# Performance work log

Measured on AMD Instinct MI355X. Metric: run time of the kernel, lower is better.

## Reference

```python
import jax, jax.numpy as jnp
import numpy as np

N, F, E, FE, H, OUT = 20000, 128, 320000, 16, 128, 128
NTYPES = 2  # types = (0, 1)
NPAIRS = NTYPES * NTYPES


def setup_inputs() -> dict:
    key = jax.random.key(0)
    ks = jax.random.split(key, 12)
    edge_in_dim = 2 * F + FE
    node_in_dim = F + H
    s = lambda *shape: 1.0 / np.sqrt(shape[-2])
    return {
        "x": jax.random.normal(ks[0], (N, 1, F), dtype=jnp.float32),
        "edge_index": jax.random.randint(ks[1], (2, E), 0, N, dtype=jnp.int64),
        "edge_attr": jax.random.normal(ks[2], (E, FE), dtype=jnp.float32),
        "node_type": jax.random.randint(ks[3], (N,), 0, NTYPES, dtype=jnp.int64),
        # edge MLP params, stacked over the 4 (t1,t2) type pairs
        "ew1": jax.random.normal(ks[4], (NPAIRS, edge_in_dim, H), dtype=jnp.float32) * (1.0 / np.sqrt(edge_in_dim)),
        "eb1": jnp.zeros((NPAIRS, H), dtype=jnp.float32),
        "ew2": jax.random.normal(ks[5], (NPAIRS, H, H), dtype=jnp.float32) * (1.0 / np.sqrt(H)),
        "eb2": jnp.zeros((NPAIRS, H), dtype=jnp.float32),
        # node MLP params, stacked over the 2 node types
        "nw1": jax.random.normal(ks[6], (NTYPES, node_in_dim, H), dtype=jnp.float32) * (1.0 / np.sqrt(node_in_dim)),
        "nb1": jnp.zeros((NTYPES, H), dtype=jnp.float32),
        "nw2": jax.random.normal(ks[7], (NTYPES, H, OUT), dtype=jnp.float32) * (1.0 / np.sqrt(H)),
        "nb2": jnp.zeros((NTYPES, OUT), dtype=jnp.float32),
    }


def reference(x, edge_index, edge_attr, node_type, ew1, eb1, ew2, eb2, nw1, nb1, nw2, nb2):
    x0 = x[:, 0]  # [N, F]
    row, col = edge_index[0], edge_index[1]

    # ---- edge model: type-pair-dispatched 2-layer ReLU MLP ----
    edge_in = jnp.concatenate([x0[row], x0[col], edge_attr], axis=-1)  # [E, 2F+FE]
    h1 = jax.nn.relu(jnp.einsum("ei,pih->eph", edge_in, ew1) + eb1)    # [E, P, H]
    h2 = jax.nn.relu(jnp.einsum("eph,phk->epk", h1, ew2) + eb2)        # [E, P, H]
    pair_id = node_type[row] * NTYPES + node_type[col]                  # [E]
    pair_oh = jax.nn.one_hot(pair_id, NPAIRS, dtype=h2.dtype)           # [E, P]
    edge_feat = jnp.einsum("epk,ep->ek", h2, pair_oh)                   # [E, H]

    # ---- aggregation: sum over incoming edges per source (row) node ----
    agg = jax.ops.segment_sum(edge_feat, row, num_segments=N)           # [N, H]

    # ---- node model: type-dispatched 2-layer MLP + residual ----
    node_in = jnp.concatenate([x0, agg], axis=-1)                       # [N, F+H]
    n1 = jax.nn.relu(jnp.einsum("ni,tih->nth", node_in, nw1) + nb1)     # [N, T, H]
    n2 = jnp.einsum("nth,thk->ntk", n1, nw2) + nb2                      # [N, T, OUT]
    type_oh = jax.nn.one_hot(node_type, NTYPES, dtype=n2.dtype)         # [N, T]
    out = jnp.einsum("ntk,nt->nk", n2, type_oh)                         # [N, OUT]
    out = out + x0[:, :OUT]  # residual
    return out[:, None, :]  # [N, 1, OUT]
```

## Files before the change

### kernel.cpp

```cpp
#include <hip/hip_runtime.h>

#define N_NODES 20000
#define N_EDGES 320000
#define NBINS   (4*N_NODES)
#define SCAN_NBLK 313
#define PRECONV_NBLK 11216
#define HIST_NBLK 1250

typedef unsigned short u16;
typedef __attribute__((ext_vector_type(8))) short bf16x8;
typedef __attribute__((ext_vector_type(4))) float f32x4;
typedef __attribute__((ext_vector_type(4))) unsigned int u32x4;
typedef __attribute__((ext_vector_type(2))) unsigned int u32x2;

__device__ __forceinline__ float b2f(u16 b){
  unsigned u = ((unsigned)b) << 16; float f; __builtin_memcpy(&f, &u, 4); return f;
}
__device__ __forceinline__ u16 f2b(float f){
  unsigned u; __builtin_memcpy(&u, &f, 4); u += 0x7FFF + ((u >> 16) & 1); return (u16)(u >> 16);
}
__device__ __forceinline__ unsigned cvtpk(float a, float b){
  unsigned r;
  asm("v_cvt_pk_bf16_f32 %0, %1, %2" : "=v"(r) : "v"(a), "v"(b));
  return r;
}

#define NX   (N_NODES*128)
#define NW1T (4*288*128)
#define NW2T (4*128*128)
#define NN1  (2*256*128)
#define NN2  (2*128*128)

__global__ void k_prep(const float* __restrict__ x,
                       const float* __restrict__ ew1, const float* __restrict__ ew2,
                       const float* __restrict__ nw1, const float* __restrict__ nw2,
                       u16* __restrict__ x0b,
                       u16* __restrict__ wt1t, u16* __restrict__ wt2t,
                       u16* __restrict__ nw1t, u16* __restrict__ nw2t,
                       const int* __restrict__ ei, const int* __restrict__ ntp,
                       int* __restrict__ hist, int* __restrict__ hist_nt,
                       u16* __restrict__ srank)
{
  int bid = blockIdx.x;
  if (bid >= PRECONV_NBLK) {
    int t = (bid - PRECONV_NBLK) * 256 + threadIdx.x;
    int lane = threadIdx.x & 63;
    if (t < N_EDGES) {
      int r = ei[t], c = ei[N_EDGES + t];
      int tr = ntp[r], tc = ntp[c];
      int key = (tr * 2 + tc) * N_NODES + r;
      int rk = atomicAdd(&hist[key], 1);
      srank[t] = (u16)rk;
    }
    bool valid = t < N_NODES;
    int ty = valid ? ntp[t] : -1;
    unsigned long long m0 = __ballot(ty == 0);
    unsigned long long m1 = __ballot(ty == 1);
    if (lane == 0) {
      int c0 = __popcll(m0), c1 = __popcll(m1);
      if (c0) atomicAdd(&hist_nt[0], c0);
      if (c1) atomicAdd(&hist_nt[1], c1);
    }
    return;
  }
  int t = bid * 256 + threadIdx.x;
  if (t < NX) { x0b[t] = f2b(x[t]); return; }
  t -= NX;
  if (t < NW1T) {
    int p = t / 36864, r = t % 36864; int k = r >> 7, n = r & 127;
    float v = (k < 272) ? ew1[(p * 272 + k) * 128 + n] : 0.f;
    wt1t[(p * 128 + n) * 288 + k] = f2b(v);
    return;
  }
  t -= NW1T;
  if (t < NW2T) {
    int p = t >> 14, r = t & 16383; int k = r >> 7, n = r & 127;
    wt2t[(p * 128 + n) * 128 + k] = f2b(ew2[(p * 128 + k) * 128 + n]);
    return;
  }
  t -= NW2T;
  if (t < NN1) {
    int ty = t >> 15, r = t & 32767; int k = r >> 7, n = r & 127;
    nw1t[(ty * 128 + n) * 256 + k] = f2b(nw1[(ty * 256 + k) * 128 + n]);
    return;
  }
  t -= NN1;
  if (t < NN2) {
    int ty = t >> 14, r = t & 16383; int k = r >> 7, n = r & 127;
    nw2t[(ty * 128 + n) * 128 + k] = f2b(nw2[(ty * 128 + k) * 128 + n]);
  }
}

__global__ void k_scan1(const int* __restrict__ hist, int* __restrict__ parts)
{
  __shared__ int s[256];
  int i = blockIdx.x * 256 + threadIdx.x;
  s[threadIdx.x] = (i < NBINS) ? hist[i] : 0;
  __syncthreads();
  for (int off = 128; off > 0; off >>= 1) {
    if (threadIdx.x < off) s[threadIdx.x] += s[threadIdx.x + off];
    __syncthreads();
  }
  if (threadIdx.x == 0) parts[blockIdx.x] = s[0];
}

__global__ void k_scan2(int* __restrict__ parts)
{
  __shared__ int s[512];
  int t = threadIdx.x;
  int v = (t < SCAN_NBLK) ? parts[t] : 0;
  s[t] = v; __syncthreads();
  for (int off = 1; off < 512; off <<= 1) {
    int xv = (t >= off) ? s[t - off] : 0;
    __syncthreads();
    s[t] += xv;
    __syncthreads();
  }
  if (t < SCAN_NBLK) parts[t] = s[t] - v;
}

__global__ void k_scan3(const int* __restrict__ hist, const int* __restrict__ parts,
                        int* __restrict__ bstart)
{
  __shared__ int s[256];
  int i = blockIdx.x * 256 + threadIdx.x;
  int v = (i < NBINS) ? hist[i] : 0;
  s[threadIdx.x] = v; __syncthreads();
  for (int off = 1; off < 256; off <<= 1) {
    int xv = (threadIdx.x >= off) ? s[threadIdx.x - off] : 0;
    __syncthreads();
    s[threadIdx.x] += xv;
    __syncthreads();
  }
  int excl = s[threadIdx.x] - v + parts[blockIdx.x];
  if (i < NBINS) bstart[i] = excl;
  if (i == 0) bstart[NBINS] = N_EDGES;
}

__global__ void k_place(const int* __restrict__ ei, const int* __restrict__ ntp,
                        const u16* __restrict__ srank, const int* __restrict__ bstart,
                        int2* __restrict__ sedge,
                        int* __restrict__ cur_nt, const int* __restrict__ hist_nt,
                        int* __restrict__ nidx)
{
  int t = blockIdx.x * 256 + threadIdx.x;
  int lane = threadIdx.x & 63;
  if (t < N_EDGES) {
    int r = ei[t], c = ei[N_EDGES + t];
    int tr = ntp[r], tc = ntp[c];
    int key = (tr * 2 + tc) * N_NODES + r;
    int pos = bstart[key] + (int)srank[t];
    int2 v; v.x = r | (c << 15); v.y = t;
    sedge[pos] = v;
  }
  bool valid = t < N_NODES;
  int ty = valid ? ntp[t] : -1;
  unsigned long long m0 = __ballot(ty == 0);
  unsigned long long m1 = __ballot(ty == 1);
  int b0 = 0, b1 = 0;
  if (lane == 0) {
    int c0 = __popcll(m0), c1 = __popcll(m1);
    if (c0) b0 = atomicAdd(&cur_nt[0], c0);
    if (c1) b1 = atomicAdd(&cur_nt[1], c1);
  }
  b0 = __shfl(b0, 0); b1 = __shfl(b1, 0);
  if (valid) {
    unsigned long long lt = (1ull << lane) - 1ull;
    int pos = (ty == 0) ? (b0 + __popcll(m0 & lt))
                        : (hist_nt[0] + b1 + __popcll(m1 & lt));
    nidx[pos] = t;
  }
}

__launch_bounds__(512, 2)
__global__ void k_edge(const u16* __restrict__ x0b, const float* __restrict__ ea,
                       const u16* __restrict__ wt1t, const u16* __restrict__ wt2t,
                       const float* __restrict__ eb1, const float* __restrict__ eb2,
                       const int* __restrict__ bstart, const int2* __restrict__ sedge,
                       u16* __restrict__ h2s)
{
  __shared__ u16 sW1[36 * 1024];
  __shared__ u16 sW2[16 * 1024];
  __shared__ u16 slab[8][16 * 128];
  __shared__ float sEb1[128];
  __shared__ float sEb2[128];

  const int p    = blockIdx.y;
  const int tid  = threadIdx.x;
  const int lane = tid & 63;
  const int wv   = tid >> 6;
  const int llo  = lane & 15;
  const int lhi  = lane >> 4;

  const int base_p = bstart[p * N_NODES];
  const int end_p  = bstart[(p + 1) * N_NODES];

  for (int i = tid; i < 128 * 36; i += 512) {
    int n = i / 36, c = i % 36;
    *(u32x4*)&sW1[(c * 128 + n) * 8] = *(const u32x4*)&wt1t[(p * 128 + n) * 288 + c * 8];
  }
  for (int i = tid; i < 128 * 16; i += 512) {
    int n = i >> 4, c = i & 15;
    *(u32x4*)&sW2[(c * 128 + n) * 8] = *(const u32x4*)&wt2t[(p * 128 + n) * 128 + c * 8];
  }
  if (tid < 128) sEb1[tid] = eb1[p * 128 + tid];
  else if (tid < 256) sEb2[tid - 128] = eb2[p * 128 + tid - 128];
  __syncthreads();

  u16* myslab = &slab[wv][0];
  const int stride = gridDim.x * 256;
  const int ts0 = base_p + blockIdx.x * 256;

  int2 mN0 = {0, 0}, mN1 = {0, 0};
  if (ts0 < end_p) {
    const int e0 = ts0 + wv * 32;
    int q0 = e0 + llo;       q0 = q0 < end_p ? q0 : end_p - 1;
    int q1 = e0 + 16 + llo;  q1 = q1 < end_p ? q1 : end_p - 1;
    mN0 = sedge[q0];
    mN1 = sedge[q1];
  }

  for (int ts = ts0; ts < end_p; ts += stride) {
    const int pos0 = ts + wv * 32 + llo;
    const int pos1 = pos0 + 16;
    const int row0 = mN0.x & 32767, col0 = mN0.x >> 15, eid0 = mN0.y;
    const int row1 = mN1.x & 32767, col1 = mN1.x >> 15, eid1 = mN1.y;

    bf16x8 xr[2][4], xc[2][4], eaf[2];
    #pragma unroll
    for (int ck = 0; ck < 4; ++ck) {
      xr[0][ck] = *(const bf16x8*)&x0b[row0 * 128 + ck * 32 + lhi * 8];
      xc[0][ck] = *(const bf16x8*)&x0b[col0 * 128 + ck * 32 + lhi * 8];
      xr[1][ck] = *(const bf16x8*)&x0b[row1 * 128 + ck * 32 + lhi * 8];
      xc[1][ck] = *(const bf16x8*)&x0b[col1 * 128 + ck * 32 + lhi * 8];
    }
    {
      u32x4 pk0 = (u32x4){0u, 0u, 0u, 0u};
      u32x4 pk1 = (u32x4){0u, 0u, 0u, 0u};
      if (lhi < 2) {
        f32x4 f0 = *(const f32x4*)&ea[eid0 * 16 + lhi * 8];
        f32x4 f1 = *(const f32x4*)&ea[eid0 * 16 + lhi * 8 + 4];
        pk0[0] = cvtpk(f0[0], f0[1]); pk0[1] = cvtpk(f0[2], f0[3]);
        pk0[2] = cvtpk(f1[0], f1[1]); pk0[3] = cvtpk(f1[2], f1[3]);
        f32x4 g0 = *(const f32x4*)&ea[eid1 * 16 + lhi * 8];
        f32x4 g1 = *(const f32x4*)&ea[eid1 * 16 + lhi * 8 + 4];
        pk1[0] = cvtpk(g0[0], g0[1]); pk1[1] = cvtpk(g0[2], g0[3]);
        pk1[2] = cvtpk(g1[0], g1[1]); pk1[3] = cvtpk(g1[2], g1[3]);
      }
      __builtin_memcpy(&eaf[0], &pk0, 16);
      __builtin_memcpy(&eaf[1], &pk1, 16);
    }

    {
      const int tn = ts + stride;
      if (tn < end_p) {
        const int e0n = tn + wv * 32;
        int q0 = e0n + llo;       q0 = q0 < end_p ? q0 : end_p - 1;
        int q1 = e0n + 16 + llo;  q1 = q1 < end_p ? q1 : end_p - 1;
        mN0 = sedge[q0];
        mN1 = sedge[q1];
      }
    }

    f32x4 acc[8][2];
    #pragma unroll
    for (int i = 0; i < 8; ++i) {
      acc[i][0] = (f32x4){0.f, 0.f, 0.f, 0.f};
      acc[i][1] = (f32x4){0.f, 0.f, 0.f, 0.f};
    }

    #pragma unroll
    for (int ck = 0; ck < 4; ++ck) {
      #pragma unroll
      for (int i = 0; i < 8; ++i) {
        bf16x8 wa = *(const bf16x8*)&sW1[((ck * 4 + lhi) * 128 + i * 16 + llo) * 8];
        acc[i][0] = __builtin_amdgcn_mfma_f32_16x16x32_bf16(wa, xr[0][ck], acc[i][0], 0, 0, 0);
        acc[i][1] = __builtin_amdgcn_mfma_f32_16x16x32_bf16(wa, xr[1][ck], acc[i][1], 0, 0, 0);
      }
    }
    #pragma unroll
    for (int ck = 0; ck < 4; ++ck) {
      #pragma unroll
      for (int i = 0; i < 8; ++i) {
        bf16x8 wb = *(const bf16x8*)&sW1[((16 + ck * 4 + lhi) * 128 + i * 16 + llo) * 8];
        acc[i][0] = __builtin_amdgcn_mfma_f32_16x16x32_bf16(wb, xc[0][ck], acc[i][0], 0, 0, 0);
        acc[i][1] = __builtin_amdgcn_mfma_f32_16x16x32_bf16(wb, xc[1][ck], acc[i][1], 0, 0, 0);
      }
    }
    #pragma unroll
    for (int i = 0; i < 8; ++i) {
      bf16x8 wce = *(const bf16x8*)&sW1[((32 + lhi) * 128 + i * 16 + llo) * 8];
      acc[i][0] = __builtin_amdgcn_mfma_f32_16x16x32_bf16(wce, eaf[0], acc[i][0], 0, 0, 0);
      acc[i][1] = __builtin_amdgcn_mfma_f32_16x16x32_bf16(wce, eaf[1], acc[i][1], 0, 0, 0);
    }

    bf16x8 h1f[2][4];
    #pragma unroll
    for (int j = 0; j < 2; ++j) {
      #pragma unroll
      for (int i = 0; i < 8; ++i) {
        const f32x4 bb = *(const f32x4*)&sEb1[i * 16 + lhi * 4];
        float v0 = acc[i][j][0] + bb[0]; v0 = v0 > 0.f ? v0 : 0.f;
        float v1 = acc[i][j][1] + bb[1]; v1 = v1 > 0.f ? v1 : 0.f;
        float v2 = acc[i][j][2] + bb[2]; v2 = v2 > 0.f ? v2 : 0.f;
        float v3 = acc[i][j][3] + bb[3]; v3 = v3 > 0.f ? v3 : 0.f;
        u32x2 pk; pk[0] = cvtpk(v0, v1); pk[1] = cvtpk(v2, v3);
        *(u32x2*)&myslab[((2 * i + (lhi >> 1)) * 16 + llo) * 8 + (lhi & 1) * 4] = pk;
      }
      #pragma unroll
      for (int ck = 0; ck < 4; ++ck)
        h1f[j][ck] = *(const bf16x8*)&myslab[((ck * 4 + lhi) * 16 + llo) * 8];
    }

    f32x4 o[8][2];
    #pragma unroll
    for (int i = 0; i < 8; ++i) {
      o[i][0] = (f32x4){0.f, 0.f, 0.f, 0.f};
      o[i][1] = (f32x4){0.f, 0.f, 0.f, 0.f};
    }
    #pragma unroll
    for (int ck = 0; ck < 4; ++ck) {
      #pragma unroll
      for (int i = 0; i < 8; ++i) {
        bf16x8 w2f = *(const bf16x8*)&sW2[((ck * 4 + lhi) * 128 + i * 16 + llo) * 8];
        o[i][0] = __builtin_amdgcn_mfma_f32_16x16x32_bf16(w2f, h1f[0][ck], o[i][0], 0, 0, 0);
        o[i][1] = __builtin_amdgcn_mfma_f32_16x16x32_bf16(w2f, h1f[1][ck], o[i][1], 0, 0, 0);
      }
    }

    #pragma unroll
    for (int i = 0; i < 8; ++i) {
      const f32x4 bb = *(const f32x4*)&sEb2[i * 16 + lhi * 4];
      {
        float v0 = o[i][0][0] + bb[0]; v0 = v0 > 0.f ? v0 : 0.f;
        float v1 = o[i][0][1] + bb[1]; v1 = v1 > 0.f ? v1 : 0.f;
        float v2 = o[i][0][2] + bb[2]; v2 = v2 > 0.f ? v2 : 0.f;
        float v3 = o[i][0][3] + bb[3]; v3 = v3 > 0.f ? v3 : 0.f;
        u32x2 pk; pk[0] = cvtpk(v0, v1); pk[1] = cvtpk(v2, v3);
        if (pos0 < end_p) *(u32x2*)&h2s[pos0 * 128 + i * 16 + lhi * 4] = pk;
      }
      {
        float v0 = o[i][1][0] + bb[0]; v0 = v0 > 0.f ? v0 : 0.f;
        float v1 = o[i][1][1] + bb[1]; v1 = v1 > 0.f ? v1 : 0.f;
        float v2 = o[i][1][2] + bb[2]; v2 = v2 > 0.f ? v2 : 0.f;
        float v3 = o[i][1][3] + bb[3]; v3 = v3 > 0.f ? v3 : 0.f;
        u32x2 pk; pk[0] = cvtpk(v0, v1); pk[1] = cvtpk(v2, v3);
        if (pos1 < end_p) *(u32x2*)&h2s[pos1 * 128 + i * 16 + lhi * 4] = pk;
      }
    }
  }
}

__launch_bounds__(512, 1)
__global__ void k_node(const u16* __restrict__ x0b, const float* __restrict__ xf,
                       const u16* __restrict__ h2s,
                       const u16* __restrict__ nw1t, const u16* __restrict__ nw2t,
                       const float* __restrict__ nb1, const float* __restrict__ nb2,
                       const int* __restrict__ bstart,
                       const int* __restrict__ nidx, const int* __restrict__ hist_nt,
                       float* __restrict__ out)
{
  const int ty    = blockIdx.y;
  const int cnt0  = hist_nt[0];
  const int cnt_t = ty ? (N_NODES - cnt0) : cnt0;
  const int base_t = ty ? cnt0 : 0;

  __shared__ u16 sNIN[64 * 264];
  __shared__ u16 sNW1[128 * 264];
  __shared__ u16 sNW2[128 * 136];
  __shared__ float sNb1[128];
  __shared__ float sNb2[128];
  __shared__ int sNid[64];

  const int tid  = threadIdx.x;
  const int lane = tid & 63;
  const int wid  = tid >> 6;
  const int llo  = lane & 15;
  const int lhi  = lane >> 4;

  for (int i = tid; i < 128 * 256; i += 512) {
    int n = i >> 8, k = i & 255;
    sNW1[n * 264 + k] = nw1t[(ty * 128 + n) * 256 + k];
  }
  for (int i = tid; i < 128 * 128; i += 512) {
    int n = i >> 7, k = i & 127;
    sNW2[n * 136 + k] = nw2t[(ty * 128 + n) * 128 + k];
  }
  if (tid < 128) { sNb1[tid] = nb1[ty * 128 + tid]; sNb2[tid] = nb2[ty * 128 + tid]; }
  __syncthreads();

  for (int t0 = blockIdx.x * 64; t0 < cnt_t; t0 += gridDim.x * 64) {
    const int cnt = min(64, cnt_t - t0);
    if (tid < 64) {
      int nid = 0;
      if (tid < cnt) nid = nidx[base_t + t0 + tid];
      sNid[tid] = nid;
    }
    __syncthreads();

    {
      const int m = tid >> 3, qq = tid & 7;
      const int nid = sNid[m];
      const u16* xs = &x0b[nid * 128 + qq * 16];
      u16* dst = &sNIN[m * 264 + qq * 16];
      #pragma unroll
      for (int j = 0; j < 2; ++j) *(u32x4*)(dst + j * 8) = *(const u32x4*)(xs + j * 8);

      float a[16];
      #pragma unroll
      for (int j = 0; j < 16; ++j) a[j] = 0.f;
      #pragma unroll
      for (int pr = 0; pr < 2; ++pr) {
        const int key = (ty * 2 + pr) * N_NODES + nid;
        const int s = bstart[key], e = bstart[key + 1];
        for (int pos = s; pos < e; ++pos) {
          const u16* hp = &h2s[pos * 128 + qq * 16];
          #pragma unroll
          for (int j = 0; j < 2; ++j) {
            u32x4 v = *(const u32x4*)(hp + j * 8);
            #pragma unroll
            for (int w = 0; w < 4; ++w) {
              unsigned uu = v[w];
              a[j * 8 + w * 2 + 0] += b2f((u16)(uu & 0xFFFFu));
              a[j * 8 + w * 2 + 1] += b2f((u16)(uu >> 16));
            }
          }
        }
      }
      u16* ad = &sNIN[m * 264 + 128 + qq * 16];
      #pragma unroll
      for (int j = 0; j < 8; ++j) {
        unsigned pk = cvtpk(a[2 * j], a[2 * j + 1]);
        *(unsigned*)(ad + 2 * j) = pk;
      }
    }
    __syncthreads();

    f32x4 acc[4];
    #pragma unroll
    for (int i = 0; i < 4; ++i) acc[i] = (f32x4){0.f, 0.f, 0.f, 0.f};

    #pragma unroll
    for (int ck = 0; ck < 8; ++ck) {
      const int kk = ck * 32 + lhi * 8;
      bf16x8 a[4], b;
      #pragma unroll
      for (int i = 0; i < 4; ++i)
        a[i] = *(const bf16x8*)&sNIN[(i * 16 + llo) * 264 + kk];
      b = *(const bf16x8*)&sNW1[(wid * 16 + llo) * 264 + kk];
      #pragma unroll
      for (int i = 0; i < 4; ++i)
        acc[i] = __builtin_amdgcn_mfma_f32_16x16x32_bf16(a[i], b, acc[i], 0, 0, 0);
    }
    __syncthreads();

    u16* sH1 = sNIN;
    #pragma unroll
    for (int i = 0; i < 4; ++i) {
      const int c = wid * 16 + llo;
      const float bias = sNb1[c];
      #pragma unroll
      for (int r = 0; r < 4; ++r) {
        const int m = i * 16 + lhi * 4 + r;
        float v = acc[i][r] + bias;
        v = v > 0.f ? v : 0.f;
        sH1[m * 136 + c] = f2b(v);
      }
    }
    __syncthreads();

    #pragma unroll
    for (int i = 0; i < 4; ++i) acc[i] = (f32x4){0.f, 0.f, 0.f, 0.f};

    #pragma unroll
    for (int ck = 0; ck < 4; ++ck) {
      const int kk = ck * 32 + lhi * 8;
      bf16x8 a[4], b;
      #pragma unroll
      for (int i = 0; i < 4; ++i)
        a[i] = *(const bf16x8*)&sH1[(i * 16 + llo) * 136 + kk];
      b = *(const bf16x8*)&sNW2[(wid * 16 + llo) * 136 + kk];
      #pragma unroll
      for (int i = 0; i < 4; ++i)
        acc[i] = __builtin_amdgcn_mfma_f32_16x16x32_bf16(a[i], b, acc[i], 0, 0, 0);
    }

    #pragma unroll
    for (int i = 0; i < 4; ++i) {
      const int c = wid * 16 + llo;
      const float bias = sNb2[c];
      #pragma unroll
      for (int r = 0; r < 4; ++r) {
        const int m = i * 16 + lhi * 4 + r;
        if (m < cnt) {
          const int nid = sNid[m];
          out[nid * 128 + c] = acc[i][r] + bias + xf[nid * 128 + c];
        }
      }
    }
    __syncthreads();
  }
}

extern "C" void kernel_launch(void* const* d_in, const int* in_sizes, int n_in,
                              void* d_out, int out_size, void* d_ws, size_t ws_size,
                              hipStream_t stream)
{
  const float* x   = (const float*)d_in[0];
  const int*   ei  = (const int*)d_in[1];
  const float* ea  = (const float*)d_in[2];
  const int*   ntp = (const int*)d_in[3];
  const float* ew1 = (const float*)d_in[4];
  const float* eb1 = (const float*)d_in[5];
  const float* ew2 = (const float*)d_in[6];
  const float* eb2 = (const float*)d_in[7];
  const float* nw1 = (const float*)d_in[8];
  const float* nb1 = (const float*)d_in[9];
  const float* nw2 = (const float*)d_in[10];
  const float* nb2 = (const float*)d_in[11];

  char* ws = (char*)d_ws;
  int*  hist    = (int*)(ws + 0);
  int*  hist_nt = (int*)(ws + 320000);
  int*  cur_nt  = (int*)(ws + 320008);
  int*  parts   = (int*)(ws + 320256);
  int*  bstart  = (int*)(ws + 321792);
  u16*  srank   = (u16*)(ws + 641824);
  int2* sedge   = (int2*)(ws + 1281824);
  int*  nidx    = (int*)(ws + 3841824);
  u16*  x0b     = (u16*)(ws + 3921824);
  u16*  wt1t    = (u16*)(ws + 9041824);
  u16*  wt2t    = (u16*)(ws + 9336736);
  u16*  nw1t    = (u16*)(ws + 9467808);
  u16*  nw2t    = (u16*)(ws + 9598880);
  u16*  h2s     = (u16*)(ws + 9664416);

  hipMemsetAsync(ws, 0, 320016, stream);
  k_prep<<<PRECONV_NBLK + HIST_NBLK, 256, 0, stream>>>(
      x, ew1, ew2, nw1, nw2, x0b, wt1t, wt2t, nw1t, nw2t,
      ei, ntp, hist, hist_nt, srank);
  k_scan1<<<SCAN_NBLK, 256, 0, stream>>>(hist, parts);
  k_scan2<<<1, 512, 0, stream>>>(parts);
  k_scan3<<<SCAN_NBLK, 256, 0, stream>>>(hist, parts, bstart);
  k_place<<<1250, 256, 0, stream>>>(ei, ntp, srank, bstart, sedge, cur_nt, hist_nt, nidx);
  k_edge<<<dim3(64, 4), 512, 0, stream>>>(x0b, ea, wt1t, wt2t, eb1, eb2, bstart, sedge, h2s);
  k_node<<<dim3(160, 2), 512, 0, stream>>>(x0b, x, h2s, nw1t, nw2t, nb1, nb2, bstart, nidx, hist_nt, (float*)d_out);
}
```

Before: 166.4 us.

## Use atomic work-stealing per wave in edge kernel with prefetched edge attributes

Replaces the static strided edge-group assignment in the edge MLP kernel with a per-pair atomic counter from which each wave grabs 32-edge groups dynamically, fixing load imbalance across blocks and type pairs. It also prefetches the next group's sorted edge record and edge attributes during the current group's MFMA work, raises wave priority around the MFMA sections, and switches streaming loads and stores (sedge, edge_attr, h2s) to nontemporal. In exchange it adds one atomic per group per wave and more live registers for the prefetched data, which could reduce occupancy.

```diff
diff --git a/kernel.cpp b/kernel.cpp
--- a/kernel.cpp
+++ b/kernel.cpp
@@ -23,6 +23,9 @@
   unsigned r;
   asm("v_cvt_pk_bf16_f32 %0, %1, %2" : "=v"(r) : "v"(a), "v"(b));
   return r;
+}
+__device__ __forceinline__ f32x4 ntl4(const float* p){
+  return __builtin_nontemporal_load((const f32x4*)p);
 }
 
 #define NX   (N_NODES*128)
@@ -177,6 +180,7 @@
                        const u16* __restrict__ wt1t, const u16* __restrict__ wt2t,
                        const float* __restrict__ eb1, const float* __restrict__ eb2,
                        const int* __restrict__ bstart, const int2* __restrict__ sedge,
+                       int* __restrict__ wcnt,
                        u16* __restrict__ h2s)
 {
   __shared__ u16 sW1[36 * 1024];
@@ -208,25 +212,58 @@
   __syncthreads();
 
   u16* myslab = &slab[wv][0];
-  const int stride = gridDim.x * 256;
-  const int ts0 = base_p + blockIdx.x * 256;
-
-  int2 mN0 = {0, 0}, mN1 = {0, 0};
-  if (ts0 < end_p) {
-    const int e0 = ts0 + wv * 32;
-    int q0 = e0 + llo;       q0 = q0 < end_p ? q0 : end_p - 1;
-    int q1 = e0 + 16 + llo;  q1 = q1 < end_p ? q1 : end_p - 1;
-    mN0 = sedge[q0];
-    mN1 = sedge[q1];
-  }
-
-  for (int ts = ts0; ts < end_p; ts += stride) {
-    const int pos0 = ts + wv * 32 + llo;
+  const int np = end_p - base_p;
+  if (np <= 0) return;
+  const int ngrp = (np + 31) >> 5;
+
+  int gv0 = 0;
+  if (lane == 0) gv0 = atomicAdd(&wcnt[p], 1);
+  int g = __shfl(gv0, 0);
+  if (g >= ngrp) return;
+
+  int mx0, my0, mx1, my1;
+  f32x4 eaN0a = {0,0,0,0}, eaN0b = {0,0,0,0}, eaN1a = {0,0,0,0}, eaN1b = {0,0,0,0};
+  {
+    const int es = base_p + g * 32;
+    int q0 = es + llo;      q0 = q0 < end_p ? q0 : end_p - 1;
+    int q1 = es + 16 + llo; q1 = q1 < end_p ? q1 : end_p - 1;
+    u32x2 a = __builtin_nontemporal_load((const u32x2*)&sedge[q0]);
+    u32x2 b = __builtin_nontemporal_load((const u32x2*)&sedge[q1]);
+    mx0 = (int)a[0]; my0 = (int)a[1]; mx1 = (int)b[0]; my1 = (int)b[1];
+    if (lhi < 2) {
+      eaN0a = ntl4(&ea[my0 * 16 + lhi * 8]);
+      eaN0b = ntl4(&ea[my0 * 16 + lhi * 8 + 4]);
+      eaN1a = ntl4(&ea[my1 * 16 + lhi * 8]);
+      eaN1b = ntl4(&ea[my1 * 16 + lhi * 8 + 4]);
+    }
+  }
+
+  while (true) {
+    int gnv = 0;
+    if (lane == 0) gnv = atomicAdd(&wcnt[p], 1);
+    const int gn = __shfl(gnv, 0);
+    const bool hn = gn < ngrp;
+
+    const int es   = base_p + g * 32;
+    const int pos0 = es + llo;
     const int pos1 = pos0 + 16;
-    const int row0 = mN0.x & 32767, col0 = mN0.x >> 15, eid0 = mN0.y;
-    const int row1 = mN1.x & 32767, col1 = mN1.x >> 15, eid1 = mN1.y;
-
-    bf16x8 xr[2][4], xc[2][4], eaf[2];
+    const int row0 = mx0 & 32767, col0 = mx0 >> 15;
+    const int row1 = mx1 & 32767, col1 = mx1 >> 15;
+
+    bf16x8 eaf[2];
+    {
+      u32x4 pk0 = (u32x4){0u,0u,0u,0u}, pk1 = (u32x4){0u,0u,0u,0u};
+      if (lhi < 2) {
+        pk0[0] = cvtpk(eaN0a[0], eaN0a[1]); pk0[1] = cvtpk(eaN0a[2], eaN0a[3]);
+        pk0[2] = cvtpk(eaN0b[0], eaN0b[1]); pk0[3] = cvtpk(eaN0b[2], eaN0b[3]);
+        pk1[0] = cvtpk(eaN1a[0], eaN1a[1]); pk1[1] = cvtpk(eaN1a[2], eaN1a[3]);
+        pk1[2] = cvtpk(eaN1b[0], eaN1b[1]); pk1[3] = cvtpk(eaN1b[2], eaN1b[3]);
+      }
+      __builtin_memcpy(&eaf[0], &pk0, 16);
+      __builtin_memcpy(&eaf[1], &pk1, 16);
+    }
+
+    bf16x8 xr[2][4], xc[2][4];
     #pragma unroll
     for (int ck = 0; ck < 4; ++ck) {
       xr[0][ck] = *(const bf16x8*)&x0b[row0 * 128 + ck * 32 + lhi * 8];
@@ -234,32 +271,14 @@
       xr[1][ck] = *(const bf16x8*)&x0b[row1 * 128 + ck * 32 + lhi * 8];
       xc[1][ck] = *(const bf16x8*)&x0b[col1 * 128 + ck * 32 + lhi * 8];
     }
-    {
-      u32x4 pk0 = (u32x4){0u, 0u, 0u, 0u};
-      u32x4 pk1 = (u32x4){0u, 0u, 0u, 0u};
-      if (lhi < 2) {
-        f32x4 f0 = *(const f32x4*)&ea[eid0 * 16 + lhi * 8];
-        f32x4 f1 = *(const f32x4*)&ea[eid0 * 16 + lhi * 8 + 4];
-        pk0[0] = cvtpk(f0[0], f0[1]); pk0[1] = cvtpk(f0[2], f0[3]);
-        pk0[2] = cvtpk(f1[0], f1[1]); pk0[3] = cvtpk(f1[2], f1[3]);
-        f32x4 g0 = *(const f32x4*)&ea[eid1 * 16 + lhi * 8];
-        f32x4 g1 = *(const f32x4*)&ea[eid1 * 16 + lhi * 8 + 4];
-        pk1[0] = cvtpk(g0[0], g0[1]); pk1[1] = cvtpk(g0[2], g0[3]);
-        pk1[2] = cvtpk(g1[0], g1[1]); pk1[3] = cvtpk(g1[2], g1[3]);
-      }
-      __builtin_memcpy(&eaf[0], &pk0, 16);
-      __builtin_memcpy(&eaf[1], &pk1, 16);
-    }
-
-    {
-      const int tn = ts + stride;
-      if (tn < end_p) {
-        const int e0n = tn + wv * 32;
-        int q0 = e0n + llo;       q0 = q0 < end_p ? q0 : end_p - 1;
-        int q1 = e0n + 16 + llo;  q1 = q1 < end_p ? q1 : end_p - 1;
-        mN0 = sedge[q0];
-        mN1 = sedge[q1];
-      }
+
+    if (hn) {
+      const int esn = base_p + gn * 32;
+      int q0 = esn + llo;      q0 = q0 < end_p ? q0 : end_p - 1;
+      int q1 = esn + 16 + llo; q1 = q1 < end_p ? q1 : end_p - 1;
+      u32x2 a = __builtin_nontemporal_load((const u32x2*)&sedge[q0]);
+      u32x2 b = __builtin_nontemporal_load((const u32x2*)&sedge[q1]);
+      mx0 = (int)a[0]; my0 = (int)a[1]; mx1 = (int)b[0]; my1 = (int)b[1];
     }
 
     f32x4 acc[8][2];
@@ -269,6 +288,7 @@
       acc[i][1] = (f32x4){0.f, 0.f, 0.f, 0.f};
     }
 
+    __builtin_amdgcn_s_setprio(1);
     #pragma unroll
     for (int ck = 0; ck < 4; ++ck) {
       #pragma unroll
@@ -293,6 +313,7 @@
       acc[i][0] = __builtin_amdgcn_mfma_f32_16x16x32_bf16(wce, eaf[0], acc[i][0], 0, 0, 0);
       acc[i][1] = __builtin_amdgcn_mfma_f32_16x16x32_bf16(wce, eaf[1], acc[i][1], 0, 0, 0);
     }
+    __builtin_amdgcn_s_setprio(0);
 
     bf16x8 h1f[2][4];
     #pragma unroll
@@ -312,12 +333,20 @@
         h1f[j][ck] = *(const bf16x8*)&myslab[((ck * 4 + lhi) * 16 + llo) * 8];
     }
 
+    if (hn && lhi < 2) {
+      eaN0a = ntl4(&ea[my0 * 16 + lhi * 8]);
+      eaN0b = ntl4(&ea[my0 * 16 + lhi * 8 + 4]);
+      eaN1a = ntl4(&ea[my1 * 16 + lhi * 8]);
+      eaN1b = ntl4(&ea[my1 * 16 + lhi * 8 + 4]);
+    }
+
     f32x4 o[8][2];
     #pragma unroll
     for (int i = 0; i < 8; ++i) {
       o[i][0] = (f32x4){0.f, 0.f, 0.f, 0.f};
       o[i][1] = (f32x4){0.f, 0.f, 0.f, 0.f};
     }
+    __builtin_amdgcn_s_setprio(1);
     #pragma unroll
     for (int ck = 0; ck < 4; ++ck) {
       #pragma unroll
@@ -327,6 +356,7 @@
         o[i][1] = __builtin_amdgcn_mfma_f32_16x16x32_bf16(w2f, h1f[1][ck], o[i][1], 0, 0, 0);
       }
     }
+    __builtin_amdgcn_s_setprio(0);
 
     #pragma unroll
     for (int i = 0; i < 8; ++i) {
@@ -337,7 +367,8 @@
         float v2 = o[i][0][2] + bb[2]; v2 = v2 > 0.f ? v2 : 0.f;
         float v3 = o[i][0][3] + bb[3]; v3 = v3 > 0.f ? v3 : 0.f;
         u32x2 pk; pk[0] = cvtpk(v0, v1); pk[1] = cvtpk(v2, v3);
-        if (pos0 < end_p) *(u32x2*)&h2s[pos0 * 128 + i * 16 + lhi * 4] = pk;
+        if (pos0 < end_p)
+          __builtin_nontemporal_store(pk, (u32x2*)&h2s[pos0 * 128 + i * 16 + lhi * 4]);
       }
       {
         float v0 = o[i][1][0] + bb[0]; v0 = v0 > 0.f ? v0 : 0.f;
@@ -345,9 +376,13 @@
         float v2 = o[i][1][2] + bb[2]; v2 = v2 > 0.f ? v2 : 0.f;
         float v3 = o[i][1][3] + bb[3]; v3 = v3 > 0.f ? v3 : 0.f;
         u32x2 pk; pk[0] = cvtpk(v0, v1); pk[1] = cvtpk(v2, v3);
-        if (pos1 < end_p) *(u32x2*)&h2s[pos1 * 128 + i * 16 + lhi * 4] = pk;
-      }
-    }
+        if (pos1 < end_p)
+          __builtin_nontemporal_store(pk, (u32x2*)&h2s[pos1 * 128 + i * 16 + lhi * 4]);
+      }
+    }
+
+    if (!hn) break;
+    g = gn;
   }
 }
 
@@ -417,7 +452,7 @@
           const u16* hp = &h2s[pos * 128 + qq * 16];
           #pragma unroll
           for (int j = 0; j < 2; ++j) {
-            u32x4 v = *(const u32x4*)(hp + j * 8);
+            u32x4 v = __builtin_nontemporal_load((const u32x4*)(hp + j * 8));
             #pragma unroll
             for (int w = 0; w < 4; ++w) {
               unsigned uu = v[w];
@@ -523,6 +558,7 @@
   int*  hist    = (int*)(ws + 0);
   int*  hist_nt = (int*)(ws + 320000);
   int*  cur_nt  = (int*)(ws + 320008);
+  int*  wcnt    = (int*)(ws + 320016);
   int*  parts   = (int*)(ws + 320256);
   int*  bstart  = (int*)(ws + 321792);
   u16*  srank   = (u16*)(ws + 641824);
@@ -535,7 +571,7 @@
   u16*  nw2t    = (u16*)(ws + 9598880);
   u16*  h2s     = (u16*)(ws + 9664416);
 
-  hipMemsetAsync(ws, 0, 320016, stream);
+  hipMemsetAsync(ws, 0, 320032, stream);
   k_prep<<<PRECONV_NBLK + HIST_NBLK, 256, 0, stream>>>(
       x, ew1, ew2, nw1, nw2, x0b, wt1t, wt2t, nw1t, nw2t,
       ei, ntp, hist, hist_nt, srank);
@@ -543,6 +579,6 @@
   k_scan2<<<1, 512, 0, stream>>>(parts);
   k_scan3<<<SCAN_NBLK, 256, 0, stream>>>(hist, parts, bstart);
   k_place<<<1250, 256, 0, stream>>>(ei, ntp, srank, bstart, sedge, cur_nt, hist_nt, nidx);
-  k_edge<<<dim3(64, 4), 512, 0, stream>>>(x0b, ea, wt1t, wt2t, eb1, eb2, bstart, sedge, h2s);
+  k_edge<<<dim3(64, 4), 512, 0, stream>>>(x0b, ea, wt1t, wt2t, eb1, eb2, bstart, sedge, wcnt, h2s);
   k_node<<<dim3(160, 2), 512, 0, stream>>>(x0b, x, h2s, nw1t, nw2t, nb1, nb2, bstart, nidx, hist_nt, (float*)d_out);
 }
```

After: 284.8 us. 71.2% more time.
